# Performance work log

Hardware: AMD Instinct MI355X
Metric: run time of the kernel (lower is better)

The kernel has to match this reference:

```python
import jax, jax.numpy as jnp
import numpy as np

B, S, D, H = 4, 2048, 1024, 16
HS = D // H  # head_size = 64
EPS = 1e-5


def setup_inputs() -> dict:
    key = jax.random.key(0)
    ks = jax.random.split(key, 10)
    s = 0.02
    return {
        "v": jax.random.normal(ks[0], (B, S, D), dtype=jnp.float32),
        "k": jax.random.normal(ks[1], (B, S, D), dtype=jnp.float32),
        "q": jax.random.normal(ks[2], (B, S, D), dtype=jnp.float32),
        "mask": jnp.triu(jnp.ones((S, S), dtype=bool), k=1),  # True = masked (causal)
        "ln_g": jnp.ones((D,), dtype=jnp.float32),
        "ln_b": jnp.zeros((D,), dtype=jnp.float32),
        # per-head projections, stacked: [H, D, HS]
        "Wq": jax.random.normal(ks[3], (H, D, HS), dtype=jnp.float32) * s,
        "Wk": jax.random.normal(ks[4], (H, D, HS), dtype=jnp.float32) * s,
        "Wv": jax.random.normal(ks[5], (H, D, HS), dtype=jnp.float32) * s,
        "Wp": jax.random.normal(ks[6], (D, D), dtype=jnp.float32) * s,
        "bp": jnp.zeros((D,), dtype=jnp.float32),
    }


def _layernorm(x, g, b):
    mu = jnp.mean(x, axis=-1, keepdims=True)
    var = jnp.var(x, axis=-1, keepdims=True)
    return (x - mu) * jax.lax.rsqrt(var + EPS) * g + b


def reference(v, k, q, mask, ln_g, ln_b, Wq, Wk, Wv, Wp, bp):
    v = _layernorm(v, ln_g, ln_b)
    k = _layernorm(k, ln_g, ln_b)
    q = _layernorm(q, ln_g, ln_b)
    # per-head projections: [B,S,D] x [H,D,E] -> [B,H,S,E]
    qh = jnp.einsum("bsd,hde->bhse", q, Wq)
    kh = jnp.einsum("bsd,hde->bhse", k, Wk)
    vh = jnp.einsum("bsd,hde->bhse", v, Wv)
    # NOTE: original scales by full embedding_dim C**-0.5 (not head_size)
    scale = jnp.float32(D) ** -0.5
    w = jnp.einsum("bhqe,bhke->bhqk", qh, kh) * scale
    w = jnp.where(mask, -jnp.inf, w)
    w = jax.nn.softmax(w, axis=-1)
    out = jnp.einsum("bhqk,bhke->bhqe", w, vh)  # [B,H,S,E]
    out = out.transpose(0, 2, 1, 3).reshape(B, S, D)  # concat heads
    return out @ Wp.T + bp
```

## Files before the change

### kernel.cpp

```cpp
#include <hip/hip_runtime.h>
#include <hip/hip_bf16.h>
#include <cstdint>
#include <cstddef>

#define Bq 4
#define Sq 2048
#define Dq 1024
#define Hq 16
#define HSq 64
#define Kc 1024

typedef short short8 __attribute__((ext_vector_type(8)));
typedef float f32x4 __attribute__((ext_vector_type(4)));

__device__ __forceinline__ unsigned short f2bf(float f){
  __hip_bfloat16 h = __float2bfloat16(f);
  return __builtin_bit_cast(unsigned short, h);
}

__device__ __forceinline__ float exp2hw(float x){
  float r;
  asm("v_exp_f32 %0, %1" : "=v"(r) : "v"(x));
  return r;
}
__device__ __forceinline__ unsigned cvtpk(float lo, float hi){
  unsigned r;
  asm("v_cvt_pk_bf16_f32 %0, %1, %2" : "=v"(r) : "v"(lo), "v"(hi));
  return r;
}
__device__ __forceinline__ float rcphw(float x){
  float r;
  asm("v_rcp_f32 %0, %1" : "=v"(r) : "v"(x));
  return r;
}

__device__ __forceinline__ void gl_lds16(const void* g, void* l){
  __builtin_amdgcn_global_load_lds((const __attribute__((address_space(1))) void*)(g),
                                   (__attribute__((address_space(3))) void*)(l), 16, 0, 0);
}

__global__ __launch_bounds__(256) void ln3_kernel(const float* __restrict__ v,
                                                  const float* __restrict__ k,
                                                  const float* __restrict__ q,
                                                  const float* __restrict__ g,
                                                  const float* __restrict__ bta,
                                                  short* __restrict__ vo,
                                                  short* __restrict__ ko,
                                                  short* __restrict__ qo){
  const int which = blockIdx.y;
  const float* x = (which==0) ? v : (which==1) ? k : q;
  short* out     = (which==0) ? vo : (which==1) ? ko : qo;
  const int row = blockIdx.x;
  const float* xr = x + (size_t)row * Dq;
  const int t = threadIdx.x;
  float4 vv = reinterpret_cast<const float4*>(xr)[t];
  float s  = vv.x + vv.y + vv.z + vv.w;
  float ss = vv.x*vv.x + vv.y*vv.y + vv.z*vv.z + vv.w*vv.w;
  #pragma unroll
  for (int o = 32; o >= 1; o >>= 1){ s += __shfl_xor(s, o); ss += __shfl_xor(ss, o); }
  __shared__ float red[8];
  const int wid = t >> 6;
  if ((t & 63) == 0){ red[wid] = s; red[4+wid] = ss; }
  __syncthreads();
  s  = red[0]+red[1]+red[2]+red[3];
  ss = red[4]+red[5]+red[6]+red[7];
  const float mu   = s * (1.0f/Dq);
  const float var  = ss * (1.0f/Dq) - mu*mu;
  const float rstd = rsqrtf(var + 1e-5f);
  float4 gv = reinterpret_cast<const float4*>(g)[t];
  float4 bv = reinterpret_cast<const float4*>(bta)[t];
  ushort4 o4;
  o4.x = f2bf((vv.x-mu)*rstd*gv.x + bv.x);
  o4.y = f2bf((vv.y-mu)*rstd*gv.y + bv.y);
  o4.z = f2bf((vv.z-mu)*rstd*gv.z + bv.z);
  o4.w = f2bf((vv.w-mu)*rstd*gv.w + bv.w);
  reinterpret_cast<ushort4*>(out + (size_t)row*Dq)[t] = o4;
}

__global__ __launch_bounds__(256) void cvt_kernel(const float* __restrict__ in,
                                                  short* __restrict__ out, int n4){
  int i = blockIdx.x*256 + threadIdx.x;
  if (i < n4){
    float4 v = reinterpret_cast<const float4*>(in)[i];
    ushort4 o; o.x=f2bf(v.x); o.y=f2bf(v.y); o.z=f2bf(v.z); o.w=f2bf(v.w);
    reinterpret_cast<ushort4*>(out)[i] = o;
  }
}

__global__ __launch_bounds__(256) void trcvt3_kernel(const float* __restrict__ Wq,
                                                     const float* __restrict__ Wk,
                                                     const float* __restrict__ Wv,
                                                     short* __restrict__ wqt,
                                                     short* __restrict__ wkt,
                                                     short* __restrict__ wvt){
  const int z = blockIdx.z;
  const float* Wsrc = (z==0) ? Wq : (z==1) ? Wk : Wv;
  short* Wdst       = (z==0) ? wqt : (z==1) ? wkt : wvt;
  const float scl   = (z==0) ? (0.03125f * 1.44269504f) : 1.0f;
  const int h = blockIdx.y, kt = blockIdx.x, tid = threadIdx.x;
  __shared__ short t[64][68];
  const float* src = Wsrc + ((size_t)h*Kc + (size_t)kt*64) * HSq;
  #pragma unroll
  for (int c=0;c<4;c++){
    int lin = c*256 + tid;
    int kr = lin >> 4;
    int e4 = (lin & 15) * 4;
    float4 vv = *reinterpret_cast<const float4*>(&src[(size_t)kr*HSq + e4]);
    t[e4+0][kr] = (short)f2bf(vv.x*scl);
    t[e4+1][kr] = (short)f2bf(vv.y*scl);
    t[e4+2][kr] = (short)f2bf(vv.z*scl);
    t[e4+3][kr] = (short)f2bf(vv.w*scl);
  }
  __syncthreads();
  short* dst = Wdst + (size_t)h*HSq*Kc + (size_t)kt*64;
  #pragma unroll
  for (int c=0;c<4;c++){
    int lin = c*256 + tid;
    int er = lin >> 4;
    int k4 = (lin & 15) * 4;
    ushort4 o;
    o.x = (unsigned short)t[er][k4+0];
    o.y = (unsigned short)t[er][k4+1];
    o.z = (unsigned short)t[er][k4+2];
    o.w = (unsigned short)t[er][k4+3];
    *reinterpret_cast<ushort4*>(&dst[(size_t)er*Kc + k4]) = o;
  }
}

__global__ __launch_bounds__(256) void proj3_kernel(
    const short* __restrict__ qn, const short* __restrict__ kn, const short* __restrict__ vn,
    const short* __restrict__ wqt, const short* __restrict__ wkt, const short* __restrict__ wvt,
    short* __restrict__ qh, short* __restrict__ kh, short* __restrict__ vhT)
{
  const int z = blockIdx.y;
  const short* A  = (z==0) ? qn  : (z==1) ? kn  : vn;
  const short* BT = (z==0) ? wqt : (z==1) ? wkt : wvt;

  const int bid = blockIdx.x;
  const int c8_ = bid & 7, j = bid >> 3;
  const int bm = c8_*8 + (j & 7), bn = j >> 3;
  const int m0 = bm * 128;
  const int n0c = bn * 128;
  const int tid = threadIdx.x;
  const int lane = tid & 63, w = tid >> 6;
  const int wm = w >> 1, wn = w & 1;
  const int fr = lane & 15, fg = lane >> 4;

  __shared__ short As[128*64];
  __shared__ short Bs[128*64];

  f32x4 acc[4][4] = {};

  const int rowT = tid >> 3;
  const int inb  = (tid & 7) * 16;

  for (int kt = 0; kt < Kc/64; ++kt){
    const int k0 = kt*64;
    #pragma unroll
    for (int c=0;c<4;c++){
      int row = c*32 + rowT;
      int src = inb ^ ((row & 7) << 4);
      gl_lds16((const char*)(A  + (size_t)(m0  + row)*Kc + k0) + src,
               (char*)As + c*4096 + w*1024);
      gl_lds16((const char*)(BT + (size_t)(n0c + row)*Kc + k0) + src,
               (char*)Bs + c*4096 + w*1024);
    }
    __syncthreads();
    #pragma unroll
    for (int kk=0;kk<2;kk++){
      short8 af[4], bf8[4];
      #pragma unroll
      for (int mr=0;mr<4;mr++){
        int row = wm*64 + mr*16 + fr;
        int byt = row*128 + ((kk*64 + fg*16) ^ ((row & 7) << 4));
        af[mr] = *reinterpret_cast<const short8*>((const char*)As + byt);
      }
      #pragma unroll
      for (int nr=0;nr<4;nr++){
        int row = wn*64 + nr*16 + fr;
        int byt = row*128 + ((kk*64 + fg*16) ^ ((row & 7) << 4));
        bf8[nr] = *reinterpret_cast<const short8*>((const char*)Bs + byt);
      }
      #pragma unroll
      for (int mr=0;mr<4;mr++)
        #pragma unroll
        for (int nr=0;nr<4;nr++)
          acc[mr][nr] = __builtin_amdgcn_mfma_f32_16x16x32_bf16(af[mr], bf8[nr], acc[mr][nr], 0, 0, 0);
    }
    __syncthreads();
  }

  if (z == 2){
    #pragma unroll
    for (int mr=0;mr<4;mr++){
      #pragma unroll
      for (int nr=0;nr<4;nr++){
        int col = n0c + wn*64 + nr*16 + fr;
        int h = col >> 6, e = col & 63;
        int R = m0 + wm*64 + mr*16 + fg*4;
        int bb = R >> 11, sPos = R & (Sq-1);
        uint2 o;
        o.x = cvtpk(acc[mr][nr][0], acc[mr][nr][1]);
        o.y = cvtpk(acc[mr][nr][2], acc[mr][nr][3]);
        *reinterpret_cast<uint2*>(&vhT[(((size_t)bb*Hq + h)*HSq + e)*Sq + sPos]) = o;
      }
    }
  } else {
    short* outb = z ? kh : qh;
    #pragma unroll
    for (int mr=0;mr<4;mr++){
      #pragma unroll
      for (int nr=0;nr<4;nr++){
        int col = n0c + wn*64 + nr*16 + fr;
        int h = col >> 6, e = col & 63;
        #pragma unroll
        for (int r=0;r<4;r++){
          int R = m0 + wm*64 + mr*16 + fg*4 + r;
          int bb = R >> 11, sPos = R & (Sq-1);
          outb[(((size_t)bb*Hq + h)*Sq + sPos)*HSq + e] = (short)f2bf(acc[mr][nr][r]);
        }
      }
    }
  }
}

__global__ __launch_bounds__(256) void gemmo_kernel(
    const short* __restrict__ A,
    const short* __restrict__ BT,
    const float* __restrict__ bias,
    float* __restrict__ outf)
{
  const int bid = blockIdx.x;
  const int c8_ = bid & 7, j = bid >> 3;
  const int bm = c8_*8 + (j & 7), bn = j >> 3;
  const int m0 = bm * 128;
  const int n0c = bn * 128;
  const int tid = threadIdx.x;
  const int lane = tid & 63, w = tid >> 6;
  const int wm = w >> 1, wn = w & 1;
  const int fr = lane & 15, fg = lane >> 4;

  __shared__ short As[128*64];
  __shared__ short Bs[128*64];

  f32x4 acc[4][4] = {};

  const int rowT = tid >> 3;
  const int inb  = (tid & 7) * 16;

  for (int kt = 0; kt < Kc/64; ++kt){
    const int k0 = kt*64;
    #pragma unroll
    for (int c=0;c<4;c++){
      int row = c*32 + rowT;
      int src = inb ^ ((row & 7) << 4);
      gl_lds16((const char*)(A  + (size_t)(m0  + row)*Kc + k0) + src,
               (char*)As + c*4096 + w*1024);
      gl_lds16((const char*)(BT + (size_t)(n0c + row)*Kc + k0) + src,
               (char*)Bs + c*4096 + w*1024);
    }
    __syncthreads();
    #pragma unroll
    for (int kk=0;kk<2;kk++){
      short8 af[4], bf8[4];
      #pragma unroll
      for (int mr=0;mr<4;mr++){
        int row = wm*64 + mr*16 + fr;
        int byt = row*128 + ((kk*64 + fg*16) ^ ((row & 7) << 4));
        af[mr] = *reinterpret_cast<const short8*>((const char*)As + byt);
      }
      #pragma unroll
      for (int nr=0;nr<4;nr++){
        int row = wn*64 + nr*16 + fr;
        int byt = row*128 + ((kk*64 + fg*16) ^ ((row & 7) << 4));
        bf8[nr] = *reinterpret_cast<const short8*>((const char*)Bs + byt);
      }
      #pragma unroll
      for (int mr=0;mr<4;mr++)
        #pragma unroll
        for (int nr=0;nr<4;nr++)
          acc[mr][nr] = __builtin_amdgcn_mfma_f32_16x16x32_bf16(af[mr], bf8[nr], acc[mr][nr], 0, 0, 0);
    }
    __syncthreads();
  }

  #pragma unroll
  for (int mr=0;mr<4;mr++){
    #pragma unroll
    for (int nr=0;nr<4;nr++){
      int col = n0c + wn*64 + nr*16 + fr;
      #pragma unroll
      for (int r=0;r<4;r++){
        int R = m0 + wm*64 + mr*16 + fg*4 + r;
        outf[(size_t)R*Dq + col] = acc[mr][nr][r] + bias[col];
      }
    }
  }
}

__global__ __launch_bounds__(256, 4) void attn_kernel(
    const short* __restrict__ qh, const short* __restrict__ kh,
    const short* __restrict__ vhT, short* __restrict__ attO)
{
  const int bid = blockIdx.x;
  const int qt  = 15 - (bid >> 6);
  const int g   = bid & 63;
  const int h = g & 15, b = g >> 4;
  const short* Q  = qh  + (((size_t)b*Hq + h)*Sq)*HSq;
  const short* K  = kh  + (((size_t)b*Hq + h)*Sq)*HSq;
  const short* VT = vhT + (((size_t)b*Hq + h)*HSq)*Sq;
  const int tid = threadIdx.x, w = tid >> 6, lane = tid & 63;
  const int fr = lane & 15, fg = lane >> 4;

  __shared__ short KsB[2][64*64];
  __shared__ short VtB[2][64*64];
  __shared__ short Ps[4][32][76];

  const int qbase = qt * 128;
  const int nkv = 2*qt + 2;

  const int sRow = tid >> 3;
  const int swz  = ((tid & 7) << 4) ^ ((sRow & 7) << 4);
  const char* pK = (const char*)K  + (size_t)sRow*128      + swz;
  const char* pV = (const char*)VT + (size_t)sRow*(Sq*2)   + swz;

  short8 qa[2][2];
  #pragma unroll
  for (int mr=0;mr<2;mr++){
    const int qrow = qbase + w*32 + mr*16 + fr;
    #pragma unroll
    for (int kk=0;kk<2;kk++)
      qa[mr][kk] = *reinterpret_cast<const short8*>(&Q[(size_t)qrow*HSq + kk*32 + 8*fg]);
  }

  f32x4 accO[2][4] = {};
  float lsum[2] = {0.0f, 0.0f};

  #pragma unroll
  for (int c=0;c<2;c++){
    gl_lds16(pK + c*4096,   (char*)KsB[0] + c*4096 + w*1024);
    gl_lds16(pV + c*131072, (char*)VtB[0] + c*4096 + w*1024);
  }
  __syncthreads();

  int buf = 0;
  for (int kt = 0; kt < nkv; ++kt){
    if (kt+1 < nkv){
      const char* nK = pK + (size_t)(kt+1)*8192;
      const char* nV = pV + (size_t)(kt+1)*128;
      #pragma unroll
      for (int c=0;c<2;c++){
        gl_lds16(nK + c*4096,   (char*)KsB[buf^1] + c*4096 + w*1024);
        gl_lds16(nV + c*131072, (char*)VtB[buf^1] + c*4096 + w*1024);
      }
    }

    f32x4 sfr[2][4] = {};
    __builtin_amdgcn_s_setprio(1);
    #pragma unroll
    for (int kk=0;kk<2;kk++){
      short8 kb[4];
      #pragma unroll
      for (int n0=0;n0<4;n0++){
        int row = n0*16 + fr;
        int byt = row*128 + ((((kk*4+fg) ^ (row & 7))) << 4);
        kb[n0] = *reinterpret_cast<const short8*>((const char*)KsB[buf] + byt);
      }
      #pragma unroll
      for (int mr=0;mr<2;mr++)
        #pragma unroll
        for (int n0=0;n0<4;n0++)
          sfr[mr][n0] = __builtin_amdgcn_mfma_f32_16x16x32_bf16(kb[n0], qa[mr][kk], sfr[mr][n0], 0, 0, 0);
    }
    __builtin_amdgcn_s_setprio(0);

    #pragma unroll
    for (int mr=0;mr<2;mr++){
      const int qr = qbase + w*32 + mr*16 + fr;
      const bool needmask = (kt*64 + 63) > (qbase + w*32 + mr*16);
      #pragma unroll
      for (int n0=0;n0<4;n0++){
        float p0 = exp2hw(sfr[mr][n0][0]);
        float p1 = exp2hw(sfr[mr][n0][1]);
        float p2 = exp2hw(sfr[mr][n0][2]);
        float p3 = exp2hw(sfr[mr][n0][3]);
        if (needmask){
          int kc = kt*64 + n0*16 + fg*4;
          if (kc+0 > qr) p0 = 0.0f;
          if (kc+1 > qr) p1 = 0.0f;
          if (kc+2 > qr) p2 = 0.0f;
          if (kc+3 > qr) p3 = 0.0f;
        }
        lsum[mr] += (p0+p1)+(p2+p3);
        uint2 u;
        u.x = cvtpk(p0, p1);
        u.y = cvtpk(p2, p3);
        *reinterpret_cast<uint2*>(&Ps[w][mr*16 + fr][n0*16 + fg*4]) = u;
      }
    }

    __builtin_amdgcn_s_setprio(1);
    #pragma unroll
    for (int kk=0;kk<2;kk++){
      short8 pa[2], vb[4];
      #pragma unroll
      for (int mr=0;mr<2;mr++)
        pa[mr] = *reinterpret_cast<short8*>(&Ps[w][mr*16 + fr][kk*32 + 8*fg]);
      #pragma unroll
      for (int n0=0;n0<4;n0++){
        int row = n0*16 + fr;
        int byt = row*128 + ((((kk*4+fg) ^ (row & 7))) << 4);
        vb[n0] = *reinterpret_cast<const short8*>((const char*)VtB[buf] + byt);
      }
      #pragma unroll
      for (int mr=0;mr<2;mr++)
        #pragma unroll
        for (int n0=0;n0<4;n0++)
          accO[mr][n0] = __builtin_amdgcn_mfma_f32_16x16x32_bf16(vb[n0], pa[mr], accO[mr][n0], 0, 0, 0);
    }
    __builtin_amdgcn_s_setprio(0);

    __syncthreads();
    buf ^= 1;
  }

  #pragma unroll
  for (int mr=0;mr<2;mr++){
    float l = lsum[mr];
    l += __shfl_xor(l, 16);
    l += __shfl_xor(l, 32);
    float inv = rcphw(l);
    const int qr = qbase + w*32 + mr*16 + fr;
    short* orow = attO + ((size_t)b*Sq + qr)*Dq + h*HSq;
    #pragma unroll
    for (int n0=0;n0<4;n0++){
      uint2 u;
      u.x = cvtpk(accO[mr][n0][0] * inv, accO[mr][n0][1] * inv);
      u.y = cvtpk(accO[mr][n0][2] * inv, accO[mr][n0][3] * inv);
      *reinterpret_cast<uint2*>(&orow[n0*16 + fg*4]) = u;
    }
  }
}

extern "C" void kernel_launch(void* const* d_in, const int* in_sizes, int n_in,
                              void* d_out, int out_size, void* d_ws, size_t ws_size,
                              hipStream_t stream){
  const float* v_in = (const float*)d_in[0];
  const float* k_in = (const float*)d_in[1];
  const float* q_in = (const float*)d_in[2];
  const float* ln_g = (const float*)d_in[4];
  const float* ln_b = (const float*)d_in[5];
  const float* Wq   = (const float*)d_in[6];
  const float* Wk   = (const float*)d_in[7];
  const float* Wv   = (const float*)d_in[8];
  const float* Wp   = (const float*)d_in[9];
  const float* bp   = (const float*)d_in[10];
  float* out = (float*)d_out;

  char* ws = (char*)d_ws;
  const size_t BSD  = (size_t)Bq*Sq*Dq;
  const size_t BSD2 = BSD * 2;
  short* vn  = (short*)(ws);
  short* kn  = (short*)(ws + BSD2);
  short* qn  = (short*)(ws + 2*BSD2);
  short* wqt = (short*)(ws + 3*BSD2);
  short* wkt = (short*)(ws + 3*BSD2 + 2097152);
  short* wvt = (short*)(ws + 3*BSD2 + 2*2097152);
  short* wpb = (short*)(ws + 3*BSD2 + 3*2097152);
  short* qh  = (short*)(ws + 3*BSD2 + 4*2097152);
  short* kh  = qh + BSD;
  short* vhT = kh + BSD;
  short* attO = vn;

  ln3_kernel<<<dim3(Bq*Sq, 3), 256, 0, stream>>>(v_in, k_in, q_in, ln_g, ln_b, vn, kn, qn);

  trcvt3_kernel<<<dim3(16, Hq, 3), 256, 0, stream>>>(Wq, Wk, Wv, wqt, wkt, wvt);
  cvt_kernel<<<1024, 256, 0, stream>>>(Wp, wpb, 262144);

  proj3_kernel<<<dim3(512, 3), 256, 0, stream>>>(qn, kn, vn, wqt, wkt, wvt, qh, kh, vhT);

  attn_kernel<<<1024, 256, 0, stream>>>(qh, kh, vhT, attO);

  gemmo_kernel<<<512, 256, 0, stream>>>(attO, wpb, bp, out);
}
```

Before: 182.0 us.

## Retile QKV projection GEMM to 256x256 with double-buffered LDS pipeline

```diff
diff --git a/kernel.cpp b/kernel.cpp
--- a/kernel.cpp
+++ b/kernel.cpp
@@ -127,7 +127,7 @@
   }
 }
 
-__global__ __launch_bounds__(256) void proj3_kernel(
+__global__ __launch_bounds__(512, 2) void proj3_kernel(
     const short* __restrict__ qn, const short* __restrict__ kn, const short* __restrict__ vn,
     const short* __restrict__ wqt, const short* __restrict__ wkt, const short* __restrict__ wvt,
     short* __restrict__ qh, short* __restrict__ kh, short* __restrict__ vhT)
@@ -136,68 +136,90 @@
   const short* A  = (z==0) ? qn  : (z==1) ? kn  : vn;
   const short* BT = (z==0) ? wqt : (z==1) ? wkt : wvt;
 
-  const int bid = blockIdx.x;
-  const int c8_ = bid & 7, j = bid >> 3;
-  const int bm = c8_*8 + (j & 7), bn = j >> 3;
-  const int m0 = bm * 128;
-  const int n0c = bn * 128;
+  const int i = blockIdx.x;
+  const int bm = i >> 2, bn = i & 3;
+  const int m0 = bm * 256;
+  const int n0c = bn * 256;
   const int tid = threadIdx.x;
   const int lane = tid & 63, w = tid >> 6;
-  const int wm = w >> 1, wn = w & 1;
+  const int wm = w >> 2, wn = w & 3;
   const int fr = lane & 15, fg = lane >> 4;
 
-  __shared__ short As[128*64];
-  __shared__ short Bs[128*64];
-
-  f32x4 acc[4][4] = {};
-
-  const int rowT = tid >> 3;
-  const int inb  = (tid & 7) * 16;
-
-  for (int kt = 0; kt < Kc/64; ++kt){
-    const int k0 = kt*64;
-    #pragma unroll
-    for (int c=0;c<4;c++){
-      int row = c*32 + rowT;
-      int src = inb ^ ((row & 7) << 4);
-      gl_lds16((const char*)(A  + (size_t)(m0  + row)*Kc + k0) + src,
-               (char*)As + c*4096 + w*1024);
-      gl_lds16((const char*)(BT + (size_t)(n0c + row)*Kc + k0) + src,
-               (char*)Bs + c*4096 + w*1024);
-    }
-    __syncthreads();
-    #pragma unroll
-    for (int kk=0;kk<2;kk++){
-      short8 af[4], bf8[4];
-      #pragma unroll
-      for (int mr=0;mr<4;mr++){
-        int row = wm*64 + mr*16 + fr;
-        int byt = row*128 + ((kk*64 + fg*16) ^ ((row & 7) << 4));
-        af[mr] = *reinterpret_cast<const short8*>((const char*)As + byt);
-      }
-      #pragma unroll
-      for (int nr=0;nr<4;nr++){
-        int row = wn*64 + nr*16 + fr;
-        int byt = row*128 + ((kk*64 + fg*16) ^ ((row & 7) << 4));
-        bf8[nr] = *reinterpret_cast<const short8*>((const char*)Bs + byt);
-      }
-      #pragma unroll
-      for (int mr=0;mr<4;mr++)
-        #pragma unroll
-        for (int nr=0;nr<4;nr++)
-          acc[mr][nr] = __builtin_amdgcn_mfma_f32_16x16x32_bf16(af[mr], bf8[nr], acc[mr][nr], 0, 0, 0);
-    }
-    __syncthreads();
+  __shared__ short As[2][256*64];
+  __shared__ short Bs[2][256*64];
+
+  f32x4 acc[8][4] = {};
+
+  const int l8 = lane >> 3;
+  const int sswz = ((lane & 7) ^ l8) << 4;
+  const char* aRow = (const char*)(A  + (size_t)(m0  + w*16 + l8)*Kc) + sswz;
+  const char* bRow = (const char*)(BT + (size_t)(n0c + w*16 + l8)*Kc) + sswz;
+
+  auto stage_half = [&](int buf, int kt, int hh){
+    const char* s = (hh < 2 ? aRow : bRow) + (size_t)(hh & 1)*262144 + (size_t)kt*128;
+    char* d = (char*)(hh < 2 ? (void*)As : (void*)Bs) + buf*32768 + (hh & 1)*16384 + w*2048;
+    gl_lds16(s,         d);
+    gl_lds16(s + 16384, d + 1024);
+  };
+
+  #pragma unroll
+  for (int hh=0; hh<4; ++hh) stage_half(0, 0, hh);
+
+  short8 bfr[4][2];
+  int cur = 0;
+  for (int t = 0; t < Kc/64; ++t){
+    const bool hasNext = (t < Kc/64 - 1);
+    #pragma unroll
+    for (int p=0; p<4; ++p){
+      if (hasNext) stage_half(cur^1, t+1, p);
+      if (p == 0){
+        if (hasNext) asm volatile("s_waitcnt vmcnt(2)" ::: "memory");
+        else         asm volatile("s_waitcnt vmcnt(0)" ::: "memory");
+        __builtin_amdgcn_s_barrier();
+        __builtin_amdgcn_sched_barrier(0);
+        #pragma unroll
+        for (int nr=0; nr<4; ++nr){
+          int row = wn*64 + nr*16 + fr;
+          #pragma unroll
+          for (int kk=0; kk<2; ++kk){
+            int byt = cur*32768 + row*128 + (((kk*4 + fg) ^ (row & 7)) << 4);
+            bfr[nr][kk] = *reinterpret_cast<const short8*>((const char*)Bs + byt);
+          }
+        }
+      }
+      short8 af[2][2];
+      #pragma unroll
+      for (int mm=0; mm<2; ++mm){
+        int row = wm*128 + (p*2 + mm)*16 + fr;
+        #pragma unroll
+        for (int kk=0; kk<2; ++kk){
+          int byt = cur*32768 + row*128 + (((kk*4 + fg) ^ (row & 7)) << 4);
+          af[mm][kk] = *reinterpret_cast<const short8*>((const char*)As + byt);
+        }
+      }
+      __builtin_amdgcn_s_setprio(1);
+      #pragma unroll
+      for (int kk=0; kk<2; ++kk)
+        #pragma unroll
+        for (int mm=0; mm<2; ++mm)
+          #pragma unroll
+          for (int nr=0; nr<4; ++nr)
+            acc[p*2+mm][nr] = __builtin_amdgcn_mfma_f32_16x16x32_bf16(af[mm][kk], bfr[nr][kk], acc[p*2+mm][nr], 0, 0, 0);
+      __builtin_amdgcn_s_setprio(0);
+    }
+    __builtin_amdgcn_sched_barrier(0);
+    __builtin_amdgcn_s_barrier();
+    cur ^= 1;
   }
 
   if (z == 2){
     #pragma unroll
-    for (int mr=0;mr<4;mr++){
-      #pragma unroll
-      for (int nr=0;nr<4;nr++){
+    for (int mr=0; mr<8; ++mr){
+      #pragma unroll
+      for (int nr=0; nr<4; ++nr){
         int col = n0c + wn*64 + nr*16 + fr;
         int h = col >> 6, e = col & 63;
-        int R = m0 + wm*64 + mr*16 + fg*4;
+        int R = m0 + wm*128 + mr*16 + fg*4;
         int bb = R >> 11, sPos = R & (Sq-1);
         uint2 o;
         o.x = cvtpk(acc[mr][nr][0], acc[mr][nr][1]);
@@ -208,14 +230,14 @@
   } else {
     short* outb = z ? kh : qh;
     #pragma unroll
-    for (int mr=0;mr<4;mr++){
-      #pragma unroll
-      for (int nr=0;nr<4;nr++){
+    for (int mr=0; mr<8; ++mr){
+      #pragma unroll
+      for (int nr=0; nr<4; ++nr){
         int col = n0c + wn*64 + nr*16 + fr;
         int h = col >> 6, e = col & 63;
         #pragma unroll
-        for (int r=0;r<4;r++){
-          int R = m0 + wm*64 + mr*16 + fg*4 + r;
+        for (int r=0; r<4; ++r){
+          int R = m0 + wm*128 + mr*16 + fg*4 + r;
           int bb = R >> 11, sPos = R & (Sq-1);
           outb[(((size_t)bb*Hq + h)*Sq + sPos)*HSq + e] = (short)f2bf(acc[mr][nr][r]);
         }
@@ -477,7 +499,7 @@
   trcvt3_kernel<<<dim3(16, Hq, 3), 256, 0, stream>>>(Wq, Wk, Wv, wqt, wkt, wvt);
   cvt_kernel<<<1024, 256, 0, stream>>>(Wp, wpb, 262144);
 
-  proj3_kernel<<<dim3(512, 3), 256, 0, stream>>>(qn, kn, vn, wqt, wkt, wvt, qh, kh, vhT);
+  proj3_kernel<<<dim3(128, 3), 512, 0, stream>>>(qn, kn, vn, wqt, wkt, wvt, qh, kh, vhT);
 
   attn_kernel<<<1024, 256, 0, stream>>>(qh, kh, vhT, attO);
 
```

Result: slower. 204.1 us (+12.1%).

## Pair complementary causal q-tiles per block and compute row sums via MFMA

Applied to the files above, without the earlier changes.

```diff
diff --git a/kernel.cpp b/kernel.cpp
--- a/kernel.cpp
+++ b/kernel.cpp
@@ -303,7 +303,7 @@
     const short* __restrict__ vhT, short* __restrict__ attO)
 {
   const int bid = blockIdx.x;
-  const int qt  = 15 - (bid >> 6);
+  const int jp  = bid >> 6;
   const int g   = bid & 63;
   const int h = g & 15, b = g >> 4;
   const short* Q  = qh  + (((size_t)b*Hq + h)*Sq)*HSq;
@@ -316,128 +316,137 @@
   __shared__ short VtB[2][64*64];
   __shared__ short Ps[4][32][76];
 
-  const int qbase = qt * 128;
-  const int nkv = 2*qt + 2;
-
   const int sRow = tid >> 3;
   const int swz  = ((tid & 7) << 4) ^ ((sRow & 7) << 4);
   const char* pK = (const char*)K  + (size_t)sRow*128      + swz;
   const char* pV = (const char*)VT + (size_t)sRow*(Sq*2)   + swz;
 
-  short8 qa[2][2];
+  short8 ones;
   #pragma unroll
-  for (int mr=0;mr<2;mr++){
-    const int qrow = qbase + w*32 + mr*16 + fr;
-    #pragma unroll
-    for (int kk=0;kk<2;kk++)
-      qa[mr][kk] = *reinterpret_cast<const short8*>(&Q[(size_t)qrow*HSq + kk*32 + 8*fg]);
-  }
-
-  f32x4 accO[2][4] = {};
-  float lsum[2] = {0.0f, 0.0f};
-
-  #pragma unroll
-  for (int c=0;c<2;c++){
-    gl_lds16(pK + c*4096,   (char*)KsB[0] + c*4096 + w*1024);
-    gl_lds16(pV + c*131072, (char*)VtB[0] + c*4096 + w*1024);
-  }
-  __syncthreads();
-
-  int buf = 0;
-  for (int kt = 0; kt < nkv; ++kt){
-    if (kt+1 < nkv){
-      const char* nK = pK + (size_t)(kt+1)*8192;
-      const char* nV = pV + (size_t)(kt+1)*128;
-      #pragma unroll
-      for (int c=0;c<2;c++){
-        gl_lds16(nK + c*4096,   (char*)KsB[buf^1] + c*4096 + w*1024);
-        gl_lds16(nV + c*131072, (char*)VtB[buf^1] + c*4096 + w*1024);
-      }
-    }
-
-    f32x4 sfr[2][4] = {};
-    __builtin_amdgcn_s_setprio(1);
-    #pragma unroll
-    for (int kk=0;kk<2;kk++){
-      short8 kb[4];
+  for (int i=0;i<8;i++) ones[i] = (short)0x3F80;
+
+  for (int pass = 0; pass < 2; ++pass){
+    const int qt = pass ? jp : (15 - jp);
+    const int qbase = qt * 128;
+    const int nkv = 2*qt + 2;
+
+    short8 qa[2][2];
+    #pragma unroll
+    for (int mr=0;mr<2;mr++){
+      const int qrow = qbase + w*32 + mr*16 + fr;
+      #pragma unroll
+      for (int kk=0;kk<2;kk++)
+        qa[mr][kk] = *reinterpret_cast<const short8*>(&Q[(size_t)qrow*HSq + kk*32 + 8*fg]);
+    }
+
+    f32x4 accO[2][4] = {};
+    f32x4 accL[2] = {};
+
+    #pragma unroll
+    for (int c=0;c<2;c++){
+      gl_lds16(pK + c*4096,   (char*)KsB[0] + c*4096 + w*1024);
+      gl_lds16(pV + c*131072, (char*)VtB[0] + c*4096 + w*1024);
+    }
+    __syncthreads();
+
+    for (int kt0 = 0; kt0 < nkv; kt0 += 2){
+      #pragma unroll
+      for (int u = 0; u < 2; ++u){
+        const int kt = kt0 + u;
+        const int buf = u;
+
+        if (kt+1 < nkv){
+          const char* nK = pK + (size_t)(kt+1)*8192;
+          const char* nV = pV + (size_t)(kt+1)*128;
+          #pragma unroll
+          for (int c=0;c<2;c++){
+            gl_lds16(nK + c*4096,   (char*)KsB[buf^1] + c*4096 + w*1024);
+            gl_lds16(nV + c*131072, (char*)VtB[buf^1] + c*4096 + w*1024);
+          }
+        }
+
+        f32x4 sfr[2][4] = {};
+        __builtin_amdgcn_s_setprio(1);
+        #pragma unroll
+        for (int kk=0;kk<2;kk++){
+          short8 kb[4];
+          #pragma unroll
+          for (int n0=0;n0<4;n0++){
+            int row = n0*16 + fr;
+            int byt = row*128 + ((((kk*4+fg) ^ (row & 7))) << 4);
+            kb[n0] = *reinterpret_cast<const short8*>((const char*)KsB[buf] + byt);
+          }
+          #pragma unroll
+          for (int mr=0;mr<2;mr++)
+            #pragma unroll
+            for (int n0=0;n0<4;n0++)
+              sfr[mr][n0] = __builtin_amdgcn_mfma_f32_16x16x32_bf16(kb[n0], qa[mr][kk], sfr[mr][n0], 0, 0, 0);
+        }
+        __builtin_amdgcn_s_setprio(0);
+
+        #pragma unroll
+        for (int mr=0;mr<2;mr++){
+          const int qr = qbase + w*32 + mr*16 + fr;
+          const bool needmask = (kt*64 + 63) > (qbase + w*32 + mr*16);
+          #pragma unroll
+          for (int n0=0;n0<4;n0++){
+            float p0 = exp2hw(sfr[mr][n0][0]);
+            float p1 = exp2hw(sfr[mr][n0][1]);
+            float p2 = exp2hw(sfr[mr][n0][2]);
+            float p3 = exp2hw(sfr[mr][n0][3]);
+            if (needmask){
+              int kc = kt*64 + n0*16 + fg*4;
+              if (kc+0 > qr) p0 = 0.0f;
+              if (kc+1 > qr) p1 = 0.0f;
+              if (kc+2 > qr) p2 = 0.0f;
+              if (kc+3 > qr) p3 = 0.0f;
+            }
+            uint2 u2;
+            u2.x = cvtpk(p0, p1);
+            u2.y = cvtpk(p2, p3);
+            *reinterpret_cast<uint2*>(&Ps[w][mr*16 + fr][n0*16 + fg*4]) = u2;
+          }
+        }
+
+        __builtin_amdgcn_s_setprio(1);
+        #pragma unroll
+        for (int kk=0;kk<2;kk++){
+          short8 pa[2], vb[4];
+          #pragma unroll
+          for (int mr=0;mr<2;mr++)
+            pa[mr] = *reinterpret_cast<short8*>(&Ps[w][mr*16 + fr][kk*32 + 8*fg]);
+          #pragma unroll
+          for (int n0=0;n0<4;n0++){
+            int row = n0*16 + fr;
+            int byt = row*128 + ((((kk*4+fg) ^ (row & 7))) << 4);
+            vb[n0] = *reinterpret_cast<const short8*>((const char*)VtB[buf] + byt);
+          }
+          #pragma unroll
+          for (int mr=0;mr<2;mr++){
+            #pragma unroll
+            for (int n0=0;n0<4;n0++)
+              accO[mr][n0] = __builtin_amdgcn_mfma_f32_16x16x32_bf16(vb[n0], pa[mr], accO[mr][n0], 0, 0, 0);
+            accL[mr] = __builtin_amdgcn_mfma_f32_16x16x32_bf16(ones, pa[mr], accL[mr], 0, 0, 0);
+          }
+        }
+        __builtin_amdgcn_s_setprio(0);
+
+        __syncthreads();
+      }
+    }
+
+    #pragma unroll
+    for (int mr=0;mr<2;mr++){
+      float inv = rcphw(accL[mr][0]);
+      const int qr = qbase + w*32 + mr*16 + fr;
+      short* orow = attO + ((size_t)b*Sq + qr)*Dq + h*HSq;
       #pragma unroll
       for (int n0=0;n0<4;n0++){
-        int row = n0*16 + fr;
-        int byt = row*128 + ((((kk*4+fg) ^ (row & 7))) << 4);
-        kb[n0] = *reinterpret_cast<const short8*>((const char*)KsB[buf] + byt);
-      }
-      #pragma unroll
-      for (int mr=0;mr<2;mr++)
-        #pragma unroll
-        for (int n0=0;n0<4;n0++)
-          sfr[mr][n0] = __builtin_amdgcn_mfma_f32_16x16x32_bf16(kb[n0], qa[mr][kk], sfr[mr][n0], 0, 0, 0);
-    }
-    __builtin_amdgcn_s_setprio(0);
-
-    #pragma unroll
-    for (int mr=0;mr<2;mr++){
-      const int qr = qbase + w*32 + mr*16 + fr;
-      const bool needmask = (kt*64 + 63) > (qbase + w*32 + mr*16);
-      #pragma unroll
-      for (int n0=0;n0<4;n0++){
-        float p0 = exp2hw(sfr[mr][n0][0]);
-        float p1 = exp2hw(sfr[mr][n0][1]);
-        float p2 = exp2hw(sfr[mr][n0][2]);
-        float p3 = exp2hw(sfr[mr][n0][3]);
-        if (needmask){
-          int kc = kt*64 + n0*16 + fg*4;
-          if (kc+0 > qr) p0 = 0.0f;
-          if (kc+1 > qr) p1 = 0.0f;
-          if (kc+2 > qr) p2 = 0.0f;
-          if (kc+3 > qr) p3 = 0.0f;
-        }
-        lsum[mr] += (p0+p1)+(p2+p3);
-        uint2 u;
-        u.x = cvtpk(p0, p1);
-        u.y = cvtpk(p2, p3);
-        *reinterpret_cast<uint2*>(&Ps[w][mr*16 + fr][n0*16 + fg*4]) = u;
-      }
-    }
-
-    __builtin_amdgcn_s_setprio(1);
-    #pragma unroll
-    for (int kk=0;kk<2;kk++){
-      short8 pa[2], vb[4];
-      #pragma unroll
-      for (int mr=0;mr<2;mr++)
-        pa[mr] = *reinterpret_cast<short8*>(&Ps[w][mr*16 + fr][kk*32 + 8*fg]);
-      #pragma unroll
-      for (int n0=0;n0<4;n0++){
-        int row = n0*16 + fr;
-        int byt = row*128 + ((((kk*4+fg) ^ (row & 7))) << 4);
-        vb[n0] = *reinterpret_cast<const short8*>((const char*)VtB[buf] + byt);
-      }
-      #pragma unroll
-      for (int mr=0;mr<2;mr++)
-        #pragma unroll
-        for (int n0=0;n0<4;n0++)
-          accO[mr][n0] = __builtin_amdgcn_mfma_f32_16x16x32_bf16(vb[n0], pa[mr], accO[mr][n0], 0, 0, 0);
-    }
-    __builtin_amdgcn_s_setprio(0);
-
-    __syncthreads();
-    buf ^= 1;
-  }
-
-  #pragma unroll
-  for (int mr=0;mr<2;mr++){
-    float l = lsum[mr];
-    l += __shfl_xor(l, 16);
-    l += __shfl_xor(l, 32);
-    float inv = rcphw(l);
-    const int qr = qbase + w*32 + mr*16 + fr;
-    short* orow = attO + ((size_t)b*Sq + qr)*Dq + h*HSq;
-    #pragma unroll
-    for (int n0=0;n0<4;n0++){
-      uint2 u;
-      u.x = cvtpk(accO[mr][n0][0] * inv, accO[mr][n0][1] * inv);
-      u.y = cvtpk(accO[mr][n0][2] * inv, accO[mr][n0][3] * inv);
-      *reinterpret_cast<uint2*>(&orow[n0*16 + fg*4]) = u;
+        uint2 u2;
+        u2.x = cvtpk(accO[mr][n0][0] * inv, accO[mr][n0][1] * inv);
+        u2.y = cvtpk(accO[mr][n0][2] * inv, accO[mr][n0][3] * inv);
+        *reinterpret_cast<uint2*>(&orow[n0*16 + fg*4]) = u2;
+      }
     }
   }
 }
@@ -479,7 +488,7 @@
 
   proj3_kernel<<<dim3(512, 3), 256, 0, stream>>>(qn, kn, vn, wqt, wkt, wvt, qh, kh, vhT);
 
-  attn_kernel<<<1024, 256, 0, stream>>>(qh, kh, vhT, attO);
+  attn_kernel<<<512, 256, 0, stream>>>(qh, kh, vhT, attO);
 
   gemmo_kernel<<<512, 256, 0, stream>>>(attO, wpb, bp, out);
 }
```

Result: slower. 186.3 us (+2.4%).
